# Kernel tuning notes

Measured on AMD Instinct MI355X. Metric: run time of the kernel, lower is better.

The kernel has to match this reference:

```python
import jax, jax.numpy as jnp
import numpy as np

N_OUT, N_CONS, N_AGE = 7, 20, 15
H = 256
B, T = 64, 365
D_ECO = N_CONS + N_AGE          # 35: eco+age feed the shared eco LSTM
D_BR = 1 + 3 + H                # 260: init + 3 age cols + eco LSTM output


def setup_inputs() -> dict:
    key = jax.random.key(0)
    ks = jax.random.split(key, 24)
    s = 0.05
    w = lambda k, shape: (jax.random.normal(k, shape, jnp.float32) * s)
    z = lambda shape: jnp.zeros(shape, jnp.float32)
    return {
        "inputs": jax.random.normal(ks[0], (B, T, N_CONS + N_OUT + N_AGE), jnp.float32),
        # shared eco LSTM (n_lstm_eco = 1)
        "eco_Wk": w(ks[1], (D_ECO, 4 * H)), "eco_Wr": w(ks[2], (H, 4 * H)), "eco_b": z((4 * H,)),
        # per-output data LSTMs (tanh)
        "data_Wk": w(ks[3], (N_OUT, D_BR, 4 * H)), "data_Wr": w(ks[4], (N_OUT, H, 4 * H)), "data_b": z((N_OUT, 4 * H)),
        # per-output attention LSTMs (activation='sigmoid')
        "att_Wk": w(ks[5], (N_OUT, D_BR, 4 * H)), "att_Wr": w(ks[6], (N_OUT, H, 4 * H)), "att_b": z((N_OUT, 4 * H)),
        # per-output tsOut LSTMs (return last state)
        "ts_Wk": w(ks[7], (N_OUT, H, 4 * H)), "ts_Wr": w(ks[8], (N_OUT, H, 4 * H)), "ts_b": z((N_OUT, 4 * H)),
        # per-output dense heads
        "d1_W": w(ks[9], (N_OUT, H, 256)), "d1_b": z((N_OUT, 256)),
        "d2_W": w(ks[10], (N_OUT, 256, 64)), "d2_b": z((N_OUT, 64)),
        "df_W": w(ks[11], (N_OUT, 64 + 3, 1)), "df_b": z((N_OUT, 1)),
    }


def _lstm(x, Wk, Wr, b, act):
    """Keras-style LSTM. x: [B,T,D]. Returns (all hidden [B,T,H], last hidden [B,H])."""
    Bc = x.shape[0]
    Hc = Wr.shape[0]
    xW = jnp.einsum('btd,dg->btg', x, Wk) + b      # precompute input projections

    def step(carry, xt):
        h, c = carry
        zi, zf, zg, zo = jnp.split(xt + h @ Wr, 4, axis=-1)  # Keras gate order i,f,c,o
        c = jax.nn.sigmoid(zf) * c + jax.nn.sigmoid(zi) * act(zg)
        h = jax.nn.sigmoid(zo) * act(c)
        return (h, c), h

    init = (jnp.zeros((Bc, Hc), x.dtype), jnp.zeros((Bc, Hc), x.dtype))
    (hT, _), hs = jax.lax.scan(step, init, jnp.swapaxes(xW, 0, 1))
    return jnp.swapaxes(hs, 0, 1), hT


def _branch(init_i, age_i, dWk, dWr, db, aWk, aWr, ab, tWk, tWr, tb, w1, b1, w2, b2, wf, bf, x_ecos):
    # init_i: [B,T,1], age_i: [B,T,3], x_ecos: [B,T,H] (shared)
    cur_input = jnp.concatenate([init_i, age_i, x_ecos], axis=-1)  # [B,T,260]
    data_hs, _ = _lstm(cur_input, dWk, dWr, db, jnp.tanh)
    att_hs, _ = _lstm(cur_input, aWk, aWr, ab, jax.nn.sigmoid)     # activation='sigmoid'
    _, h_last = _lstm(data_hs * att_hs, tWk, tWr, tb, jnp.tanh)    # return_sequences=False
    h = jax.nn.relu(h_last @ w1 + b1)
    h = jax.nn.relu(h @ w2 + b2)
    h = jnp.concatenate([h, cur_input[:, -1, 1:4]], axis=-1)       # append last-step age cols
    out = h @ wf + bf + cur_input[:, -1, :1]                       # residual add of last init
    return out  # [B,1]


def reference(inputs, eco_Wk, eco_Wr, eco_b, data_Wk, data_Wr, data_b,
              att_Wk, att_Wr, att_b, ts_Wk, ts_Wr, ts_b,
              d1_W, d1_b, d2_W, d2_b, df_W, df_b):
    x_init = inputs[:, :, N_CONS:N_CONS + N_OUT]                       # [B,T,7]
    x_age = inputs[:, :, N_CONS + N_OUT:N_CONS + N_OUT + N_AGE]        # [B,T,15]
    x_eco = inputs[:, :, :N_CONS]                                      # [B,T,20]

    x_ecos, _ = _lstm(jnp.concatenate([x_eco, x_age], axis=-1), eco_Wk, eco_Wr, eco_b, jnp.tanh)  # [B,T,256]

    init_i = jnp.moveaxis(x_init, 2, 0)[..., None]                     # [7,B,T,1]
    i_idx = jnp.arange(N_OUT)
    age_cols = jnp.stack([jnp.zeros_like(i_idx), i_idx + 1, i_idx + 8], axis=1)  # [7,3]
    age_i = jnp.moveaxis(x_age[:, :, age_cols], 2, 0)                  # [7,B,T,3]

    outs = jax.vmap(_branch, in_axes=(0,) * 17 + (None,))(
        init_i, age_i, data_Wk, data_Wr, data_b, att_Wk, att_Wr, att_b,
        ts_Wk, ts_Wr, ts_b, d1_W, d1_b, d2_W, d2_b, df_W, df_b, x_ecos)  # [7,B,1]
    return jnp.transpose(outs[:, :, 0])  # [B,7]
```

## Files before the change

### kernel.cpp

```cpp
#include <hip/hip_runtime.h>


#define TT 365
#define RE 4
#define RS 4

typedef short bf16x8 __attribute__((ext_vector_type(8)));
typedef float f32x4 __attribute__((ext_vector_type(4)));

__device__ __forceinline__ float b2f(unsigned short u) {
  union { unsigned u32; float f; } v; v.u32 = ((unsigned)u) << 16; return v.f;
}
__device__ __forceinline__ unsigned short f2b(float f) {
  union { float f; unsigned u32; } v; v.f = f;
  unsigned u = v.u32;
  u = u + 0x7FFFu + ((u >> 16) & 1u);
  return (unsigned short)(u >> 16);
}
__device__ __forceinline__ float sigf(float x) { return 1.0f / (1.0f + __expf(-x)); }
__device__ __forceinline__ float tanh_(float x) { return 2.0f / (1.0f + __expf(-2.0f * x)) - 1.0f; }

__device__ __forceinline__ unsigned long long ld64(const unsigned long long* p) {
  return __hip_atomic_load(p, __ATOMIC_RELAXED, __HIP_MEMORY_SCOPE_AGENT);
}
// ... 51 lines not shown
  __syncthreads();
  for (int e = tid; e < 8192; e += 256) {
    int col2 = e >> 5, ks = e & 31;
    dst[(size_t)kb * 32768 + (cc * 256 + col2) * 32 + ks] = f2b(ls[ks * 261 + col2]);
  }
}

__global__ __launch_bounds__(256) void k1_ecoxw(const float* __restrict__ inputs,
    const float* __restrict__ eco_Wk, const float* __restrict__ eco_b,
    unsigned short* __restrict__ xw_eco)
{
  __shared__ float Asl[64 * 35];
  __shared__ float Bsl[35 * 256];
  const int tg = blockIdx.x, ct = blockIdx.y, tid = threadIdx.x;
  for (int i = tid; i < 64 * 35; i += 256) {
    int b = i / 35, k = i - b * 35;
    int col = (k < 20) ? k : (k + 7);
    Asl[i] = inputs[((size_t)b * TT + tg) * 42 + col];
  }
  for (int i = tid; i < 35 * 256; i += 256) {
    int k = i >> 8, c = i & 255;
    Bsl[i] = eco_Wk[(size_t)k * 1024 + ct * 256 + c];
  }
  __syncthreads();
  const float bias = eco_b[ct * 256 + tid];
  for (int r = 0; r < 64; ++r) {
    float s = bias;
    #pragma unroll
    for (int k = 0; k < 35; ++k) s += Asl[r * 35 + k] * Bsl[k * 256 + tid];
    xw_eco[((size_t)tg * 64 + r) * 1024 + ct * 256 + tid] = f2b(s);
  }
}

__global__ __launch_bounds__(256, 1) void kP(
    const unsigned short* __restrict__ wr_swz,
    const unsigned short* __restrict__ wk_da,
    const unsigned short* __restrict__ wk_ts,
    const unsigned short* __restrict__ xw_eco,
    const float* __restrict__ inputs,
    const float* __restrict__ data_Wk, const float* __restrict__ att_Wk,
    const float* __restrict__ data_b, const float* __restrict__ att_b,
    const float* __restrict__ ts_b,
    unsigned long long* __restrict__ hE,
    unsigned long long* __restrict__ hD,
    unsigned long long* __restrict__ hsD,
    unsigned long long* __restrict__ hsA,
    unsigned long long* __restrict__ h2,
    unsigned* __restrict__ hDf, unsigned* __restrict__ h2f,
    float* __restrict__ h_last)
{
  __shared__ __align__(16) unsigned char smem[160256];
  const int tid = threadIdx.x;
  const int widx = blockIdx.x;
  const int lane = tid & 63, w = tid >> 6, c = lane & 15, grp = lane >> 4;

  if (widx < 16) {
    unsigned short* WR = (unsigned short*)smem;
    unsigned short* Hs = (unsigned short*)(smem + 81920);
    float* zsh = (float*)(smem + 102400);
    float* cst = (float*)(smem + 119296);
    const int wg = widx >> 1, bg = widx & 1;
    const unsigned short* wr_g = wr_swz + (size_t)wg * 32768;
    for (int i = tid * 8; i < 32768; i += 2048) {
      int kb = i >> 12; int rr = i & 4095; int col = rr >> 5; int ks = rr & 31;
      *(uint4*)&WR[(kb * 128 + col) * 40 + ks] = *(const uint4*)&wr_g[i];
    }
    for (int i = tid; i < 1024; i += 256) cst[i] = 0.0f;

    int xoff[16];
    #pragma unroll
    for (int rt = 0; rt < 2; ++rt)
      #pragma unroll
      for (int ct = 0; ct < 2; ++ct)
        #pragma unroll
        for (int rg = 0; rg < 4; ++rg)
          xoff[(rt * 2 + ct) * 4 + rg] =
              (bg * 32 + rt * 16 + grp * 4 + rg) * 1024 + w * 256 + wg * 32 + ct * 16 + c;
    unsigned short xv[16], xn[16];
    #pragma unroll
    for (int i = 0; i < 16; ++i) xv[i] = xw_eco[xoff[i]];
    __syncthreads();

    for (int t = 0; t < TT; ++t) {
      if (t + 1 > RE && tid < 112) {
        while ((int)ld32(&hDf[tid]) < t + 1 - RE) __builtin_amdgcn_s_sleep(2);
      }
      {
        const unsigned long long* hb = hE + (size_t)(t % RE) * 8192;
        unsigned long long v[16];
        #pragma unroll
        for (int i = 0; i < 16; ++i) {
          int m = tid + i * 256;
          v[i] = ld64(&hb[(bg * 32 + (m >> 7)) * 128 + (m & 127)]);
        }
        const unsigned tagv = (unsigned)t;
        int tries = 0;
        while (true) {
          unsigned pend = 0u;
          #pragma unroll
          for (int i = 0; i < 16; ++i)
            pend |= ((unsigned)(v[i] >> 32) != tagv) ? (1u << i) : 0u;
          if (!pend) break;
          if (++tries > 8) __builtin_amdgcn_s_sleep(1);
          #pragma unroll
          for (int i = 0; i < 16; ++i)
            if (pend & (1u << i)) {
              int m = tid + i * 256;
              v[i] = ld64(&hb[(bg * 32 + (m >> 7)) * 128 + (m & 127)]);
            }
        }
        #pragma unroll
        for (int i = 0; i < 16; ++i) {
          int m = tid + i * 256, row = m >> 7, kp = m & 127;
          *(unsigned int*)&Hs[((kp >> 4) * 32 + row) * 40 + 2 * (kp & 15)] = (unsigned int)v[i];
        }
      }
      __syncthreads();
      f32x4 acc[4];
      #pragma unroll
      for (int i = 0; i < 4; ++i)
        #pragma unroll
        for (int rg = 0; rg < 4; ++rg) acc[i][rg] = b2f(xv[i * 4 + rg]);
      if (t + 1 < TT) {
        const unsigned short* xw1 = xw_eco + (size_t)(t + 1) * 65536;
        #pragma unroll
        for (int i = 0; i < 16; ++i) xn[i] = xw1[xoff[i]];
      }
      #pragma unroll
      for (int kb = 0; kb < 8; ++kb) {
        bf16x8 a0 = *(const bf16x8*)&Hs[(kb * 32 + c) * 40 + grp * 8];
        bf16x8 a1 = *(const bf16x8*)&Hs[(kb * 32 + 16 + c) * 40 + grp * 8];
        bf16x8 b0 = *(const bf16x8*)&WR[(kb * 128 + w * 32 + c) * 40 + grp * 8];
        bf16x8 b1 = *(const bf16x8*)&WR[(kb * 128 + w * 32 + 16 + c) * 40 + grp * 8];
        acc[0] = __builtin_amdgcn_mfma_f32_16x16x32_bf16(a0, b0, acc[0], 0, 0, 0);
        acc[1] = __builtin_amdgcn_mfma_f32_16x16x32_bf16(a0, b1, acc[1], 0, 0, 0);
        acc[2] = __builtin_amdgcn_mfma_f32_16x16x32_bf16(a1, b0, acc[2], 0, 0, 0);
        acc[3] = __builtin_amdgcn_mfma_f32_16x16x32_bf16(a1, b1, acc[3], 0, 0, 0);
      }
      #pragma unroll
      for (int i = 0; i < 4; ++i) {
        int rt = i >> 1, ct = i & 1;
        #pragma unroll
        for (int rg = 0; rg < 4; ++rg)
          zsh[(rt * 16 + grp * 4 + rg) * 132 + w * 32 + ct * 16 + c] = acc[i][rg];
      }
      __syncthreads();
      {
        int row = tid >> 3, hq8 = tid & 7;
        float4 zi = *(const float4*)&zsh[row * 132 +      hq8 * 4];
        float4 zf = *(const float4*)&zsh[row * 132 + 32 + hq8 * 4];
        float4 zg = *(const float4*)&zsh[row * 132 + 64 + hq8 * 4];
        float4 zo = *(const float4*)&zsh[row * 132 + 96 + hq8 * 4];
        float4 c0 = *(const float4*)&cst[row * 32 + hq8 * 4];
        float cn0 = sigf(zf.x) * c0.x + sigf(zi.x) * tanh_(zg.x);
        float cn1 = sigf(zf.y) * c0.y + sigf(zi.y) * tanh_(zg.y);
        float cn2 = sigf(zf.z) * c0.z + sigf(zi.z) * tanh_(zg.z);
        float cn3 = sigf(zf.w) * c0.w + sigf(zi.w) * tanh_(zg.w);
        float hv0 = sigf(zo.x) * tanh_(cn0);
        float hv1 = sigf(zo.y) * tanh_(cn1);
        float hv2 = sigf(zo.z) * tanh_(cn2);
        float hv3 = sigf(zo.w) * tanh_(cn3);
        *(float4*)&cst[row * 32 + hq8 * 4] = make_float4(cn0, cn1, cn2, cn3);
        unsigned long long* ho = hE + (size_t)((t + 1) % RE) * 8192
                               + (bg * 32 + row) * 128 + wg * 16 + hq8 * 2;
        st64(&ho[0], tag2(t + 1, hv0, hv1));
        st64(&ho[1], tag2(t + 1, hv2, hv3));
      }
      __syncthreads();
      #pragma unroll
      for (int i = 0; i < 16; ++i) xv[i] = xn[i];
    }
  } else if (widx < 128) {
    unsigned short* WR = (unsigned short*)smem;
    unsigned short* Hs = (unsigned short*)(smem + 81920);
    float* zsh = (float*)(smem + 122880);
    float* a_sp = (float*)(smem + 156672);
    float* b_sp = (float*)(smem + 157696);
    float* bias_s = (float*)(smem + 159744);
    const int q = widx - 16, l1 = q >> 3, colwg = q & 7, br = l1 >> 1;
    const bool act_sig = (l1 & 1);
    const unsigned short* wr_g = wr_swz + ((size_t)(1 + l1) * 8 + colwg) * 32768;
    for (int i = tid * 8; i < 32768; i += 2048) {
      int kb = i >> 12; int rr = i & 4095; int col = rr >> 5; int ks = rr & 31;
      *(uint4*)&WR[(kb * 128 + col) * 40 + ks] = *(const uint4*)&wr_g[i];
    }
    bf16x8 wkf[16];
    const unsigned short* wk = wk_da + (size_t)l1 * 262144;
    #pragma unroll
    for (int kb = 0; kb < 8; ++kb)
      #pragma unroll
      for (int ct = 0; ct < 2; ++ct) {
        int col = w * 256 + colwg * 32 + ct * 16 + c;
        wkf[kb * 2 + ct] = *(const bf16x8*)&wk[kb * 32768 + col * 32 + grp * 8];
      }
    const float* spWk = (act_sig ? att_Wk : data_Wk) + (size_t)br * 266240;
    for (int i = tid; i < 512; i += 256) {
      int j = i >> 7, colL = i & 127;
      int gcol = (colL >> 5) * 256 + colwg * 32 + (colL & 31);
      b_sp[i] = spWk[(size_t)j * 1024 + gcol];
    }
    if (tid < 128) {
      int gcol = (tid >> 5) * 256 + colwg * 32 + (tid & 31);
      bias_s[tid] = (act_sig ? att_b : data_b)[br * 1024 + gcol];
    }
    float creg[8];
    #pragma unroll
    for (int j = 0; j < 8; ++j) creg[j] = 0.0f;
    unsigned long long* hDl = hD + (size_t)l1 * 2 * 8192;
    unsigned long long* ring = (act_sig ? hsA : hsD) + (size_t)br * RS * 8192;
    __syncthreads();

    for (int t = 0; t < TT; ++t) {
      if (t + 1 > RS && tid < 16) {
        while ((int)ld32(&h2f[br * 16 + tid]) < t + 1 - RS) __builtin_amdgcn_s_sleep(2);
      }
      if (tid < 64) {
        const float* ip = inputs + ((size_t)tid * TT + t) * 42;
        a_sp[tid * 4 + 0] = ip[20 + br];
        a_sp[tid * 4 + 1] = ip[27];
        a_sp[tid * 4 + 2] = ip[27 + br + 1];
        a_sp[tid * 4 + 3] = ip[27 + br + 8];
      }
      const unsigned long long* he = hE + (size_t)((t + 1) % RE) * 8192;
      const unsigned long long* ho = hDl + (size_t)(t & 1) * 8192;
      unsigned long long ve[32], vh[32];
      #pragma unroll
      for (int i = 0; i < 32; ++i) ve[i] = ld64(&he[tid + i * 256]);
      #pragma unroll
      for (int i = 0; i < 32; ++i) vh[i] = ld64(&ho[tid + i * 256]);
      {
        const unsigned tagv = (unsigned)(t + 1);
        int tries = 0;
        while (true) {
          unsigned long long pend = 0ull;
          #pragma unroll
          for (int i = 0; i < 32; ++i)
            pend |= ((unsigned)(ve[i] >> 32) != tagv) ? (1ull << i) : 0ull;
          if (!pend) break;
          if (++tries > 8) __builtin_amdgcn_s_sleep(1);
          #pragma unroll
          for (int i = 0; i < 32; ++i)
            if (pend & (1ull << i)) ve[i] = ld64(&he[tid + i * 256]);
        }
      }
      #pragma unroll
      for (int i = 0; i < 32; ++i) {
        int m = tid + i * 256, row = m >> 7, kp = m & 127;
        *(unsigned int*)&Hs[((kp >> 4) * 64 + row) * 40 + 2 * (kp & 15)] = (unsigned int)ve[i];
      }
      __syncthreads();
      f32x4 acc[8] = {};
      #pragma unroll
      for (int kb = 0; kb < 8; ++kb) {
        bf16x8 a[4];
        #pragma unroll
        for (int rt = 0; rt < 4; ++rt)
          a[rt] = *(const bf16x8*)&Hs[(kb * 64 + rt * 16 + c) * 40 + grp * 8];
        #pragma unroll
        for (int rt = 0; rt < 4; ++rt)
          #pragma unroll
          for (int ct = 0; ct < 2; ++ct)
            acc[rt * 2 + ct] = __builtin_amdgcn_mfma_f32_16x16x32_bf16(a[rt], wkf[kb * 2 + ct], acc[rt * 2 + ct], 0, 0, 0);
      }
      #pragma unroll
      for (int i = 0; i < 8; ++i) {
        int rt = i >> 1, ct2 = i & 1;
        #pragma unroll
        for (int rg = 0; rg < 4; ++rg) {
          int row = rt * 16 + grp * 4 + rg;
          int colL = w * 32 + ct2 * 16 + c;
          acc[i][rg] += bias_s[colL]
                      + a_sp[row * 4 + 0] * b_sp[colL]       + a_sp[row * 4 + 1] * b_sp[128 + colL]
                      + a_sp[row * 4 + 2] * b_sp[256 + colL] + a_sp[row * 4 + 3] * b_sp[384 + colL];
        }
      }
      {
        const unsigned tagv = (unsigned)t;
        int tries = 0;
        while (true) {
          unsigned long long pend = 0ull;
          #pragma unroll
          for (int i = 0; i < 32; ++i)
            pend |= ((unsigned)(vh[i] >> 32) != tagv) ? (1ull << i) : 0ull;
          if (!pend) break;
          if (++tries > 8) __builtin_amdgcn_s_sleep(1);
          #pragma unroll
          for (int i = 0; i < 32; ++i)
            if (pend & (1ull << i)) vh[i] = ld64(&ho[tid + i * 256]);
        }
      }
      __syncthreads();
      #pragma unroll
      for (int i = 0; i < 32; ++i) {
        int m = tid + i * 256, row = m >> 7, kp = m & 127;
        *(unsigned int*)&Hs[((kp >> 4) * 64 + row) * 40 + 2 * (kp & 15)] = (unsigned int)vh[i];
      }
      __syncthreads();
      #pragma unroll
      for (int kb = 0; kb < 8; ++kb) {
        bf16x8 a[4]; bf16x8 b[2];
        #pragma unroll
        for (int rt = 0; rt < 4; ++rt)
          a[rt] = *(const bf16x8*)&Hs[(kb * 64 + rt * 16 + c) * 40 + grp * 8];
        #pragma unroll
        for (int ct = 0; ct < 2; ++ct)
          b[ct] = *(const bf16x8*)&WR[(kb * 128 + w * 32 + ct * 16 + c) * 40 + grp * 8];
        #pragma unroll
        for (int rt = 0; rt < 4; ++rt)
          #pragma unroll
          for (int ct = 0; ct < 2; ++ct)
            acc[rt * 2 + ct] = __builtin_amdgcn_mfma_f32_16x16x32_bf16(a[rt], b[ct], acc[rt * 2 + ct], 0, 0, 0);
      }
      #pragma unroll
      for (int i = 0; i < 8; ++i) {
        int rt = i >> 1, ct2 = i & 1;
        #pragma unroll
        for (int rg = 0; rg < 4; ++rg)
          zsh[(rt * 16 + grp * 4 + rg) * 132 + w * 32 + ct2 * 16 + c] = acc[i][rg];
      }
      __syncthreads();
      {
        unsigned long long* hon = hDl + (size_t)((t + 1) & 1) * 8192;
        unsigned long long* rs = ring + (size_t)(t % RS) * 8192;
        #pragma unroll
        for (int it = 0; it < 2; ++it) {
          int m = tid + it * 256, row = m >> 3, hq8 = m & 7;
          float4 zi = *(const float4*)&zsh[row * 132 +      hq8 * 4];
          float4 zf = *(const float4*)&zsh[row * 132 + 32 + hq8 * 4];
          float4 zg = *(const float4*)&zsh[row * 132 + 64 + hq8 * 4];
          float4 zo = *(const float4*)&zsh[row * 132 + 96 + hq8 * 4];
          float g0 = act_sig ? sigf(zg.x) : tanh_(zg.x);
          float g1 = act_sig ? sigf(zg.y) : tanh_(zg.y);
          float g2 = act_sig ? sigf(zg.z) : tanh_(zg.z);
          float g3 = act_sig ? sigf(zg.w) : tanh_(zg.w);
          float cn0 = sigf(zf.x) * creg[it * 4 + 0] + sigf(zi.x) * g0;
          float cn1 = sigf(zf.y) * creg[it * 4 + 1] + sigf(zi.y) * g1;
          float cn2 = sigf(zf.z) * creg[it * 4 + 2] + sigf(zi.z) * g2;
          float cn3 = sigf(zf.w) * creg[it * 4 + 3] + sigf(zi.w) * g3;
          float hv0 = sigf(zo.x) * (act_sig ? sigf(cn0) : tanh_(cn0));
          float hv1 = sigf(zo.y) * (act_sig ? sigf(cn1) : tanh_(cn1));
          float hv2 = sigf(zo.z) * (act_sig ? sigf(cn2) : tanh_(cn2));
          float hv3 = sigf(zo.w) * (act_sig ? sigf(cn3) : tanh_(cn3));
          creg[it * 4 + 0] = cn0; creg[it * 4 + 1] = cn1;
          creg[it * 4 + 2] = cn2; creg[it * 4 + 3] = cn3;
          int kp = colwg * 16 + hq8 * 2;
          unsigned long long w0 = tag2(t + 1, hv0, hv1);
          unsigned long long w1 = tag2(t + 1, hv2, hv3);
          st64(&hon[row * 128 + kp], w0);
          st64(&hon[row * 128 + kp + 1], w1);
          st64(&rs[row * 128 + kp], w0);
          st64(&rs[row * 128 + kp + 1], w1);
        }
      }
      __builtin_amdgcn_s_waitcnt(0);
      __syncthreads();
      if (tid == 0) st32(&hDf[q], (unsigned)(t + 1));
    }
  } else {
    unsigned short* WR = (unsigned short*)smem;
    unsigned short* Hs = (unsigned short*)(smem + 81920);
    float* zsh = (float*)(smem + 102400);
    float* bias_s = (float*)(smem + 119296);
    const int r = widx - 128, d = r >> 4, sub = r & 15, colwg = sub >> 1, bg = sub & 1;
    const unsigned short* wr_g = wr_swz + ((size_t)(15 + d) * 8 + colwg) * 32768;
    for (int i = tid * 8; i < 32768; i += 2048) {
      int kb = i >> 12; int rr = i & 4095; int col = rr >> 5; int ks = rr & 31;
      *(uint4*)&WR[(kb * 128 + col) * 40 + ks] = *(const uint4*)&wr_g[i];
    }
    bf16x8 wkf[16];
    const unsigned short* wk = wk_ts + (size_t)d * 262144;
    #pragma unroll
    for (int kb = 0; kb < 8; ++kb)
      #pragma unroll
      for (int ct = 0; ct < 2; ++ct) {
        int col = w * 256 + colwg * 32 + ct * 16 + c;
        wkf[kb * 2 + ct] = *(const bf16x8*)&wk[kb * 32768 + col * 32 + grp * 8];
      }
    if (tid < 128) {
      int gcol = (tid >> 5) * 256 + colwg * 32 + (tid & 31);
      bias_s[tid] = ts_b[d * 1024 + gcol];
    }
    float creg[4] = {0.0f, 0.0f, 0.0f, 0.0f};
    const unsigned long long* rD = hsD + (size_t)d * RS * 8192;
    const unsigned long long* rA = hsA + (size_t)d * RS * 8192;
    unsigned long long* h2d = h2 + (size_t)d * 2 * 8192;
    __syncthreads();

    for (int t = 0; t < TT; ++t) {
      const unsigned long long* sd = rD + (size_t)(t % RS) * 8192;
      const unsigned long long* sa = rA + (size_t)(t % RS) * 8192;
      const unsigned long long* ho = h2d + (size_t)(t & 1) * 8192;
      unsigned long long vd[16], va[16], vh[16];
      int idx16[16];
      #pragma unroll
      for (int i = 0; i < 16; ++i) {
        int m = tid + i * 256;
        idx16[i] = (bg * 32 + (m >> 7)) * 128 + (m & 127);
      }
      #pragma unroll
      for (int i = 0; i < 16; ++i) vd[i] = ld64(&sd[idx16[i]]);
      #pragma unroll
      for (int i = 0; i < 16; ++i) va[i] = ld64(&sa[idx16[i]]);
      #pragma unroll
      for (int i = 0; i < 16; ++i) vh[i] = ld64(&ho[idx16[i]]);
      {
        const unsigned tagv = (unsigned)(t + 1);
        int tries = 0;
        while (true) {
          unsigned pend = 0u;
          #pragma unroll
          for (int i = 0; i < 16; ++i) {
            pend |= ((unsigned)(vd[i] >> 32) != tagv) ? (1u << i) : 0u;
            pend |= ((unsigned)(va[i] >> 32) != tagv) ? (0x10000u << i) : 0u;
          }
          if (!pend) break;
          if (++tries > 8) __builtin_amdgcn_s_sleep(1);
          #pragma unroll
          for (int i = 0; i < 16; ++i) {
            if (pend & (1u << i)) vd[i] = ld64(&sd[idx16[i]]);
            if (pend & (0x10000u << i)) va[i] = ld64(&sa[idx16[i]]);
          }
        }
      }
      #pragma unroll
      for (int i = 0; i < 16; ++i) {
        int m = tid + i * 256, row = m >> 7, kp = m & 127;
        unsigned dl = (unsigned)vd[i], al = (unsigned)va[i];
        float p0 = b2f((unsigned short)dl) * b2f((unsigned short)al);
        float p1 = b2f((unsigned short)(dl >> 16)) * b2f((unsigned short)(al >> 16));
        unsigned pv = (unsigned)f2b(p0) | ((unsigned)f2b(p1) << 16);
        *(unsigned int*)&Hs[((kp >> 4) * 32 + row) * 40 + 2 * (kp & 15)] = pv;
      }
      __syncthreads();
      f32x4 acc[4] = {};
      #pragma unroll
      for (int kb = 0; kb < 8; ++kb) {
        bf16x8 a0 = *(const bf16x8*)&Hs[(kb * 32 + c) * 40 + grp * 8];
        bf16x8 a1 = *(const bf16x8*)&Hs[(kb * 32 + 16 + c) * 40 + grp * 8];
        acc[0] = __builtin_amdgcn_mfma_f32_16x16x32_bf16(a0, wkf[kb * 2 + 0], acc[0], 0, 0, 0);
        acc[1] = __builtin_amdgcn_mfma_f32_16x16x32_bf16(a0, wkf[kb * 2 + 1], acc[1], 0, 0, 0);
        acc[2] = __builtin_amdgcn_mfma_f32_16x16x32_bf16(a1, wkf[kb * 2 + 0], acc[2], 0, 0, 0);
        acc[3] = __builtin_amdgcn_mfma_f32_16x16x32_bf16(a1, wkf[kb * 2 + 1], acc[3], 0, 0, 0);
      }
      #pragma unroll
      for (int i = 0; i < 4; ++i) {
        int ct2 = i & 1;
        #pragma unroll
        for (int rg = 0; rg < 4; ++rg)
          acc[i][rg] += bias_s[w * 32 + ct2 * 16 + c];
      }
      {
        const unsigned tagv = (unsigned)t;
        int tries = 0;
        while (true) {
          unsigned pend = 0u;
          #pragma unroll
          for (int i = 0; i < 16; ++i)
            pend |= ((unsigned)(vh[i] >> 32) != tagv) ? (1u << i) : 0u;
          if (!pend) break;
          if (++tries > 8) __builtin_amdgcn_s_sleep(1);
          #pragma unroll
          for (int i = 0; i < 16; ++i)
            if (pend & (1u << i)) vh[i] = ld64(&ho[idx16[i]]);
        }
      }
      __syncthreads();
      #pragma unroll
      for (int i = 0; i < 16; ++i) {
        int m = tid + i * 256, row = m >> 7, kp = m & 127;
        *(unsigned int*)&Hs[((kp >> 4) * 32 + row) * 40 + 2 * (kp & 15)] = (unsigned int)vh[i];
      }
      __syncthreads();
      #pragma unroll
      for (int kb = 0; kb < 8; ++kb) {
        bf16x8 a0 = *(const bf16x8*)&Hs[(kb * 32 + c) * 40 + grp * 8];
        bf16x8 a1 = *(const bf16x8*)&Hs[(kb * 32 + 16 + c) * 40 + grp * 8];
        bf16x8 b0 = *(const bf16x8*)&WR[(kb * 128 + w * 32 + c) * 40 + grp * 8];
        bf16x8 b1 = *(const bf16x8*)&WR[(kb * 128 + w * 32 + 16 + c) * 40 + grp * 8];
        acc[0] = __builtin_amdgcn_mfma_f32_16x16x32_bf16(a0, b0, acc[0], 0, 0, 0);
        acc[1] = __builtin_amdgcn_mfma_f32_16x16x32_bf16(a0, b1, acc[1], 0, 0, 0);
        acc[2] = __builtin_amdgcn_mfma_f32_16x16x32_bf16(a1, b0, acc[2], 0, 0, 0);
        acc[3] = __builtin_amdgcn_mfma_f32_16x16x32_bf16(a1, b1, acc[3], 0, 0, 0);
      }
      #pragma unroll
      for (int i = 0; i < 4; ++i) {
        int rt = i >> 1, ct2 = i & 1;
        #pragma unroll
        for (int rg = 0; rg < 4; ++rg)
          zsh[(rt * 16 + grp * 4 + rg) * 132 + w * 32 + ct2 * 16 + c] = acc[i][rg];
      }
      __syncthreads();
      {
        int row = tid >> 3, hq8 = tid & 7;
        float4 zi = *(const float4*)&zsh[row * 132 +      hq8 * 4];
        float4 zf = *(const float4*)&zsh[row * 132 + 32 + hq8 * 4];
        float4 zg = *(const float4*)&zsh[row * 132 + 64 + hq8 * 4];
        float4 zo = *(const float4*)&zsh[row * 132 + 96 + hq8 * 4];
        float cn0 = sigf(zf.x) * creg[0] + sigf(zi.x) * tanh_(zg.x);
        float cn1 = sigf(zf.y) * creg[1] + sigf(zi.y) * tanh_(zg.y);
        float cn2 = sigf(zf.z) * creg[2] + sigf(zi.z) * tanh_(zg.z);
        float cn3 = sigf(zf.w) * creg[3] + sigf(zi.w) * tanh_(zg.w);
        float hv0 = sigf(zo.x) * tanh_(cn0);
        float hv1 = sigf(zo.y) * tanh_(cn1);
        float hv2 = sigf(zo.z) * tanh_(cn2);
        float hv3 = sigf(zo.w) * tanh_(cn3);
        creg[0] = cn0; creg[1] = cn1; creg[2] = cn2; creg[3] = cn3;
        unsigned long long* hn = h2d + (size_t)((t + 1) & 1) * 8192
                               + (bg * 32 + row) * 128 + colwg * 16 + hq8 * 2;
        st64(&hn[0], tag2(t + 1, hv0, hv1));
        st64(&hn[1], tag2(t + 1, hv2, hv3));
        if (t == TT - 1) {
          *(float4*)&h_last[(size_t)d * 16384 + (bg * 32 + row) * 256 + colwg * 32 + hq8 * 4]
              = make_float4(hv0, hv1, hv2, hv3);
        }
      }
      __builtin_amdgcn_s_waitcnt(0);
      __syncthreads();
      if (tid == 0) st32(&h2f[d * 16 + sub], (unsigned)(t + 1));
    }
  }
}

__global__ __launch_bounds__(256) void k7_d1(const float* __restrict__ h_last,
    const float* __restrict__ d1_W, const float* __restrict__ d1_b, float* __restrict__ d1o)
{
  __shared__ float Asl[64 * 256];
  __shared__ float Bsl[256 * 64];
  const int nt = blockIdx.x, br = blockIdx.y, tid = threadIdx.x;
  const float* hl = h_last + (size_t)br * 16384;
  for (int i = tid; i < 16384; i += 256) Asl[i] = hl[i];
  const float* wp = d1_W + (size_t)br * 65536 + nt * 64;
  for (int i = tid; i < 16384; i += 256) {
    int k = i >> 6, cl = i & 63;
    Bsl[i] = wp[(size_t)k * 256 + cl];
  }
  __syncthreads();
  const int cl = tid & 63, rq = tid >> 6;
  float s[16];
  const float bias = d1_b[br * 256 + nt * 64 + cl];
  #pragma unroll
  for (int i = 0; i < 16; ++i) s[i] = bias;
  for (int k = 0; k < 256; ++k) {
    float bv = Bsl[k * 64 + cl];
    #pragma unroll
    for (int i = 0; i < 16; ++i) s[i] += Asl[(rq * 16 + i) * 256 + k] * bv;
  }
  #pragma unroll
  for (int i = 0; i < 16; ++i)
    d1o[(size_t)br * 16384 + (rq * 16 + i) * 256 + nt * 64 + cl] = fmaxf(s[i], 0.0f);
}

// ... 49 lines not shown
  const float* att_Wk  = (const float*)d_in[7];
  const float* att_Wr  = (const float*)d_in[8];
  const float* att_b   = (const float*)d_in[9];
  const float* ts_Wk   = (const float*)d_in[10];
  const float* ts_Wr   = (const float*)d_in[11];
  const float* ts_b    = (const float*)d_in[12];
  const float* d1_W    = (const float*)d_in[13];
  const float* d1_b    = (const float*)d_in[14];
  const float* d2_W    = (const float*)d_in[15];
  const float* d2_b    = (const float*)d_in[16];
  const float* df_W    = (const float*)d_in[17];
  const float* df_b    = (const float*)d_in[18];

  char* ws = (char*)d_ws;
  size_t off = 0;
  auto take = [&](size_t bytes) -> void* {
    void* p = ws + off;
    off += (bytes + 255) & ~(size_t)255;
    return p;
  };
  unsigned short* wr_swz = (unsigned short*)take((size_t)22 * 262144 * 2);
  unsigned short* wk_da  = (unsigned short*)take((size_t)14 * 262144 * 2);
  unsigned short* wk_ts  = (unsigned short*)take((size_t)7  * 262144 * 2);
  unsigned short* xw_eco = (unsigned short*)take((size_t)TT * 65536 * 2);
  float*          h_last = (float*)take((size_t)7 * 16384 * 4);
  float*          d1o    = (float*)take((size_t)7 * 16384 * 4);
  size_t sync_begin = off;
  unsigned long long* hE  = (unsigned long long*)take((size_t)RE * 8192 * 8);
  unsigned long long* hD  = (unsigned long long*)take((size_t)14 * 2 * 8192 * 8);
  unsigned long long* hsD = (unsigned long long*)take((size_t)7 * RS * 8192 * 8);
  unsigned long long* hsA = (unsigned long long*)take((size_t)7 * RS * 8192 * 8);
  unsigned long long* h2  = (unsigned long long*)take((size_t)7 * 2 * 8192 * 8);
  unsigned* hDf = (unsigned*)take(112 * 4);
  unsigned* h2f = (unsigned*)take(112 * 4);
  size_t sync_bytes = off - sync_begin;
  if (off > ws_size) return;

  hipMemsetAsync(ws + sync_begin, 0, sync_bytes, stream);
  k0a_wr<<<dim3(8, 8, 22), 256, 0, stream>>>(eco_Wr, data_Wr, att_Wr, ts_Wr, wr_swz);
  k0b_wk<<<dim3(4, 8, 21), 256, 0, stream>>>(data_Wk, att_Wk, ts_Wk, wk_da, wk_ts);
  k1_ecoxw<<<dim3(TT, 4), 256, 0, stream>>>(inputs, eco_Wk, eco_b, xw_eco);
  kP<<<240, 256, 0, stream>>>(wr_swz, wk_da, wk_ts, xw_eco, inputs,
                              data_Wk, att_Wk, data_b, att_b, ts_b,
                              hE, hD, hsD, hsA, h2, hDf, h2f, h_last);
  k7_d1<<<dim3(4, 7), 256, 0, stream>>>(h_last, d1_W, d1_b, d1o);
  k8_head<<<7, 256, 0, stream>>>(d1o, d2_W, d2_b, df_W, df_b, inputs, (float*)d_out);
}
```

Before: 3.904 ms.

## Merge batch-half workgroups into 512-thread blocks in persistent LSTM kernel

The persistent recurrence kernel now runs 512-thread workgroups. Each block covers both 32-row batch halves that were previously handled by separate blocks, so each recurrent weight slice is loaded into shared memory once instead of twice. The grid shrinks from 240 to 176 blocks, and the per-step readiness flags for the ts LSTM drop from 16 to 8 per branch. The eco cell state moves into registers and one block barrier per eco step is dropped. In exchange, each block carries more waves and larger barrier groups, which may lengthen per-step barrier latency on the serial critical path.

```diff
diff --git a/kernel.cpp b/kernel.cpp
--- a/kernel.cpp
+++ b/kernel.cpp
@@ -107,7 +107,7 @@
   }
 }
 
-__global__ __launch_bounds__(256, 1) void kP(
+__global__ __launch_bounds__(512, 2) void kP(
     const unsigned short* __restrict__ wr_swz,
     const unsigned short* __restrict__ wk_da,
     const unsigned short* __restrict__ wk_ts,
@@ -127,21 +127,20 @@
   __shared__ __align__(16) unsigned char smem[160256];
   const int tid = threadIdx.x;
   const int widx = blockIdx.x;
-  const int lane = tid & 63, w = tid >> 6, c = lane & 15, grp = lane >> 4;
-
-  if (widx < 16) {
+  const int lane = tid & 63, w = (tid >> 6) & 3, c = lane & 15, grp = lane >> 4;
+  const int half = tid >> 8, tid256 = tid & 255;
+  const int crow = tid >> 3, chq = tid & 7;
+
+  if (widx < 8) {
     unsigned short* WR = (unsigned short*)smem;
     unsigned short* Hs = (unsigned short*)(smem + 81920);
-    float* zsh = (float*)(smem + 102400);
-    float* cst = (float*)(smem + 119296);
-    const int wg = widx >> 1, bg = widx & 1;
+    float* zsh = (float*)(smem + 122880);
+    const int wg = widx;
     const unsigned short* wr_g = wr_swz + (size_t)wg * 32768;
-    for (int i = tid * 8; i < 32768; i += 2048) {
+    for (int i = tid * 8; i < 32768; i += 4096) {
       int kb = i >> 12; int rr = i & 4095; int col = rr >> 5; int ks = rr & 31;
       *(uint4*)&WR[(kb * 128 + col) * 40 + ks] = *(const uint4*)&wr_g[i];
     }
-    for (int i = tid; i < 1024; i += 256) cst[i] = 0.0f;
-
     int xoff[16];
     #pragma unroll
     for (int rt = 0; rt < 2; ++rt)
@@ -150,10 +149,11 @@
         #pragma unroll
         for (int rg = 0; rg < 4; ++rg)
           xoff[(rt * 2 + ct) * 4 + rg] =
-              (bg * 32 + rt * 16 + grp * 4 + rg) * 1024 + w * 256 + wg * 32 + ct * 16 + c;
+              (half * 32 + rt * 16 + grp * 4 + rg) * 1024 + w * 256 + wg * 32 + ct * 16 + c;
     unsigned short xv[16], xn[16];
     #pragma unroll
     for (int i = 0; i < 16; ++i) xv[i] = xw_eco[xoff[i]];
+    float cs0 = 0.0f, cs1 = 0.0f, cs2 = 0.0f, cs3 = 0.0f;
     __syncthreads();
 
     for (int t = 0; t < TT; ++t) {
@@ -165,8 +165,8 @@
         unsigned long long v[16];
         #pragma unroll
         for (int i = 0; i < 16; ++i) {
-          int m = tid + i * 256;
-          v[i] = ld64(&hb[(bg * 32 + (m >> 7)) * 128 + (m & 127)]);
+          int m = tid256 + i * 256;
+          v[i] = ld64(&hb[(half * 32 + (m >> 7)) * 128 + (m & 127)]);
         }
         const unsigned tagv = (unsigned)t;
         int tries = 0;
@@ -180,14 +180,15 @@
           #pragma unroll
           for (int i = 0; i < 16; ++i)
             if (pend & (1u << i)) {
-              int m = tid + i * 256;
-              v[i] = ld64(&hb[(bg * 32 + (m >> 7)) * 128 + (m & 127)]);
+              int m = tid256 + i * 256;
+              v[i] = ld64(&hb[(half * 32 + (m >> 7)) * 128 + (m & 127)]);
             }
         }
         #pragma unroll
         for (int i = 0; i < 16; ++i) {
-          int m = tid + i * 256, row = m >> 7, kp = m & 127;
-          *(unsigned int*)&Hs[((kp >> 4) * 32 + row) * 40 + 2 * (kp & 15)] = (unsigned int)v[i];
+          int m = tid256 + i * 256, rl = m >> 7, kp = m & 127;
+          *(unsigned int*)&Hs[half * 10240 + ((kp >> 4) * 32 + rl) * 40 + 2 * (kp & 15)]
+              = (unsigned int)v[i];
         }
       }
       __syncthreads();
@@ -203,8 +204,8 @@
       }
       #pragma unroll
       for (int kb = 0; kb < 8; ++kb) {
-        bf16x8 a0 = *(const bf16x8*)&Hs[(kb * 32 + c) * 40 + grp * 8];
-        bf16x8 a1 = *(const bf16x8*)&Hs[(kb * 32 + 16 + c) * 40 + grp * 8];
+        bf16x8 a0 = *(const bf16x8*)&Hs[half * 10240 + (kb * 32 + c) * 40 + grp * 8];
+        bf16x8 a1 = *(const bf16x8*)&Hs[half * 10240 + (kb * 32 + 16 + c) * 40 + grp * 8];
         bf16x8 b0 = *(const bf16x8*)&WR[(kb * 128 + w * 32 + c) * 40 + grp * 8];
         bf16x8 b1 = *(const bf16x8*)&WR[(kb * 128 + w * 32 + 16 + c) * 40 + grp * 8];
         acc[0] = __builtin_amdgcn_mfma_f32_16x16x32_bf16(a0, b0, acc[0], 0, 0, 0);
@@ -217,45 +218,42 @@
         int rt = i >> 1, ct = i & 1;
         #pragma unroll
         for (int rg = 0; rg < 4; ++rg)
-          zsh[(rt * 16 + grp * 4 + rg) * 132 + w * 32 + ct * 16 + c] = acc[i][rg];
+          zsh[(half * 32 + rt * 16 + grp * 4 + rg) * 132 + w * 32 + ct * 16 + c] = acc[i][rg];
       }
       __syncthreads();
       {
-        int row = tid >> 3, hq8 = tid & 7;
-        float4 zi = *(const float4*)&zsh[row * 132 +      hq8 * 4];
-        float4 zf = *(const float4*)&zsh[row * 132 + 32 + hq8 * 4];
-        float4 zg = *(const float4*)&zsh[row * 132 + 64 + hq8 * 4];
-        float4 zo = *(const float4*)&zsh[row * 132 + 96 + hq8 * 4];
-        float4 c0 = *(const float4*)&cst[row * 32 + hq8 * 4];
-        float cn0 = sigf(zf.x) * c0.x + sigf(zi.x) * tanh_(zg.x);
-        float cn1 = sigf(zf.y) * c0.y + sigf(zi.y) * tanh_(zg.y);
-        float cn2 = sigf(zf.z) * c0.z + sigf(zi.z) * tanh_(zg.z);
-        float cn3 = sigf(zf.w) * c0.w + sigf(zi.w) * tanh_(zg.w);
+        float4 zi = *(const float4*)&zsh[crow * 132 +      chq * 4];
+        float4 zf = *(const float4*)&zsh[crow * 132 + 32 + chq * 4];
+        float4 zg = *(const float4*)&zsh[crow * 132 + 64 + chq * 4];
+        float4 zo = *(const float4*)&zsh[crow * 132 + 96 + chq * 4];
+        float cn0 = sigf(zf.x) * cs0 + sigf(zi.x) * tanh_(zg.x);
+        float cn1 = sigf(zf.y) * cs1 + sigf(zi.y) * tanh_(zg.y);
+        float cn2 = sigf(zf.z) * cs2 + sigf(zi.z) * tanh_(zg.z);
+        float cn3 = sigf(zf.w) * cs3 + sigf(zi.w) * tanh_(zg.w);
         float hv0 = sigf(zo.x) * tanh_(cn0);
         float hv1 = sigf(zo.y) * tanh_(cn1);
         float hv2 = sigf(zo.z) * tanh_(cn2);
         float hv3 = sigf(zo.w) * tanh_(cn3);
-        *(float4*)&cst[row * 32 + hq8 * 4] = make_float4(cn0, cn1, cn2, cn3);
+        cs0 = cn0; cs1 = cn1; cs2 = cn2; cs3 = cn3;
         unsigned long long* ho = hE + (size_t)((t + 1) % RE) * 8192
-                               + (bg * 32 + row) * 128 + wg * 16 + hq8 * 2;
+                               + crow * 128 + wg * 16 + chq * 2;
         st64(&ho[0], tag2(t + 1, hv0, hv1));
         st64(&ho[1], tag2(t + 1, hv2, hv3));
       }
-      __syncthreads();
       #pragma unroll
       for (int i = 0; i < 16; ++i) xv[i] = xn[i];
     }
-  } else if (widx < 128) {
+  } else if (widx < 120) {
     unsigned short* WR = (unsigned short*)smem;
     unsigned short* Hs = (unsigned short*)(smem + 81920);
     float* zsh = (float*)(smem + 122880);
     float* a_sp = (float*)(smem + 156672);
     float* b_sp = (float*)(smem + 157696);
     float* bias_s = (float*)(smem + 159744);
-    const int q = widx - 16, l1 = q >> 3, colwg = q & 7, br = l1 >> 1;
+    const int q = widx - 8, l1 = q >> 3, colwg = q & 7, br = l1 >> 1;
     const bool act_sig = (l1 & 1);
     const unsigned short* wr_g = wr_swz + ((size_t)(1 + l1) * 8 + colwg) * 32768;
-    for (int i = tid * 8; i < 32768; i += 2048) {
+    for (int i = tid * 8; i < 32768; i += 4096) {
       int kb = i >> 12; int rr = i & 4095; int col = rr >> 5; int ks = rr & 31;
       *(uint4*)&WR[(kb * 128 + col) * 40 + ks] = *(const uint4*)&wr_g[i];
     }
@@ -269,25 +267,23 @@
         wkf[kb * 2 + ct] = *(const bf16x8*)&wk[kb * 32768 + col * 32 + grp * 8];
       }
     const float* spWk = (act_sig ? att_Wk : data_Wk) + (size_t)br * 266240;
-    for (int i = tid; i < 512; i += 256) {
-      int j = i >> 7, colL = i & 127;
+    {
+      int j = tid >> 7, colL = tid & 127;
       int gcol = (colL >> 5) * 256 + colwg * 32 + (colL & 31);
-      b_sp[i] = spWk[(size_t)j * 1024 + gcol];
+      b_sp[tid] = spWk[(size_t)j * 1024 + gcol];
     }
     if (tid < 128) {
       int gcol = (tid >> 5) * 256 + colwg * 32 + (tid & 31);
       bias_s[tid] = (act_sig ? att_b : data_b)[br * 1024 + gcol];
     }
-    float creg[8];
-    #pragma unroll
-    for (int j = 0; j < 8; ++j) creg[j] = 0.0f;
+    float creg[4] = {0.0f, 0.0f, 0.0f, 0.0f};
     unsigned long long* hDl = hD + (size_t)l1 * 2 * 8192;
     unsigned long long* ring = (act_sig ? hsA : hsD) + (size_t)br * RS * 8192;
     __syncthreads();
 
     for (int t = 0; t < TT; ++t) {
-      if (t + 1 > RS && tid < 16) {
-        while ((int)ld32(&h2f[br * 16 + tid]) < t + 1 - RS) __builtin_amdgcn_s_sleep(2);
+      if (t + 1 > RS && tid < 8) {
+        while ((int)ld32(&h2f[br * 8 + tid]) < t + 1 - RS) __builtin_amdgcn_s_sleep(2);
       }
       if (tid < 64) {
         const float* ip = inputs + ((size_t)tid * TT + t) * 42;
@@ -298,51 +294,58 @@
       }
       const unsigned long long* he = hE + (size_t)((t + 1) % RE) * 8192;
       const unsigned long long* ho = hDl + (size_t)(t & 1) * 8192;
-      unsigned long long ve[32], vh[32];
-      #pragma unroll
-      for (int i = 0; i < 32; ++i) ve[i] = ld64(&he[tid + i * 256]);
-      #pragma unroll
-      for (int i = 0; i < 32; ++i) vh[i] = ld64(&ho[tid + i * 256]);
+      unsigned long long ve[16], vh[16];
+      #pragma unroll
+      for (int i = 0; i < 16; ++i) {
+        int m = tid256 + i * 256;
+        int idx = (half * 32 + (m >> 7)) * 128 + (m & 127);
+        ve[i] = ld64(&he[idx]);
+        vh[i] = ld64(&ho[idx]);
+      }
       {
         const unsigned tagv = (unsigned)(t + 1);
         int tries = 0;
         while (true) {
-          unsigned long long pend = 0ull;
-          #pragma unroll
-          for (int i = 0; i < 32; ++i)
-            pend |= ((unsigned)(ve[i] >> 32) != tagv) ? (1ull << i) : 0ull;
+          unsigned pend = 0u;
+          #pragma unroll
+          for (int i = 0; i < 16; ++i)
+            pend |= ((unsigned)(ve[i] >> 32) != tagv) ? (1u << i) : 0u;
           if (!pend) break;
           if (++tries > 8) __builtin_amdgcn_s_sleep(1);
           #pragma unroll
-          for (int i = 0; i < 32; ++i)
-            if (pend & (1ull << i)) ve[i] = ld64(&he[tid + i * 256]);
-        }
-      }
-      #pragma unroll
-      for (int i = 0; i < 32; ++i) {
-        int m = tid + i * 256, row = m >> 7, kp = m & 127;
-        *(unsigned int*)&Hs[((kp >> 4) * 64 + row) * 40 + 2 * (kp & 15)] = (unsigned int)ve[i];
-      }
-      __syncthreads();
-      f32x4 acc[8] = {};
+          for (int i = 0; i < 16; ++i)
+            if (pend & (1u << i)) {
+              int m = tid256 + i * 256;
+              ve[i] = ld64(&he[(half * 32 + (m >> 7)) * 128 + (m & 127)]);
+            }
+        }
+      }
+      #pragma unroll
+      for (int i = 0; i < 16; ++i) {
+        int m = tid256 + i * 256, rl = m >> 7, kp = m & 127;
+        *(unsigned int*)&Hs[((kp >> 4) * 64 + half * 32 + rl) * 40 + 2 * (kp & 15)]
+            = (unsigned int)ve[i];
+      }
+      __syncthreads();
+      f32x4 acc[4] = {};
       #pragma unroll
       for (int kb = 0; kb < 8; ++kb) {
-        bf16x8 a[4];
-        #pragma unroll
-        for (int rt = 0; rt < 4; ++rt)
-          a[rt] = *(const bf16x8*)&Hs[(kb * 64 + rt * 16 + c) * 40 + grp * 8];
-        #pragma unroll
-        for (int rt = 0; rt < 4; ++rt)
+        bf16x8 a[2];
+        #pragma unroll
+        for (int rt = 0; rt < 2; ++rt)
+          a[rt] = *(const bf16x8*)&Hs[(kb * 64 + half * 32 + rt * 16 + c) * 40 + grp * 8];
+        #pragma unroll
+        for (int rt = 0; rt < 2; ++rt)
           #pragma unroll
           for (int ct = 0; ct < 2; ++ct)
             acc[rt * 2 + ct] = __builtin_amdgcn_mfma_f32_16x16x32_bf16(a[rt], wkf[kb * 2 + ct], acc[rt * 2 + ct], 0, 0, 0);
       }
       #pragma unroll
-      for (int i = 0; i < 8; ++i) {
+      for (int i = 0; i < 4; ++i) {
         int rt = i >> 1, ct2 = i & 1;
         #pragma unroll
         for (int rg = 0; rg < 4; ++rg) {
-          int row = rt * 16 + grp * 4 + rg;
+          int row = half * 32 + rt * 16 + grp * 4 + rg;
           int colL = w * 32 + ct2 * 16 + c;
           acc[i][rg] += bias_s[colL]
                       + a_sp[row * 4 + 0] * b_sp[colL]       + a_sp[row * 4 + 1] * b_sp[128 + colL]
@@ -353,79 +356,78 @@
         const unsigned tagv = (unsigned)t;
         int tries = 0;
         while (true) {
-          unsigned long long pend = 0ull;
-          #pragma unroll
-          for (int i = 0; i < 32; ++i)
-            pend |= ((unsigned)(vh[i] >> 32) != tagv) ? (1ull << i) : 0ull;
+          unsigned pend = 0u;
+          #pragma unroll
+          for (int i = 0; i < 16; ++i)
+            pend |= ((unsigned)(vh[i] >> 32) != tagv) ? (1u << i) : 0u;
           if (!pend) break;
           if (++tries > 8) __builtin_amdgcn_s_sleep(1);
           #pragma unroll
-          for (int i = 0; i < 32; ++i)
-            if (pend & (1ull << i)) vh[i] = ld64(&ho[tid + i * 256]);
-        }
-      }
-      __syncthreads();
-      #pragma unroll
-      for (int i = 0; i < 32; ++i) {
-        int m = tid + i * 256, row = m >> 7, kp = m & 127;
-        *(unsigned int*)&Hs[((kp >> 4) * 64 + row) * 40 + 2 * (kp & 15)] = (unsigned int)vh[i];
+          for (int i = 0; i < 16; ++i)
+            if (pend & (1u << i)) {
+              int m = tid256 + i * 256;
+              vh[i] = ld64(&ho[(half * 32 + (m >> 7)) * 128 + (m & 127)]);
+            }
+        }
+      }
+      __syncthreads();
+      #pragma unroll
+      for (int i = 0; i < 16; ++i) {
+        int m = tid256 + i * 256, rl = m >> 7, kp = m & 127;
+        *(unsigned int*)&Hs[((kp >> 4) * 64 + half * 32 + rl) * 40 + 2 * (kp & 15)]
+            = (unsigned int)vh[i];
       }
       __syncthreads();
       #pragma unroll
       for (int kb = 0; kb < 8; ++kb) {
-        bf16x8 a[4]; bf16x8 b[2];
-        #pragma unroll
-        for (int rt = 0; rt < 4; ++rt)
-          a[rt] = *(const bf16x8*)&Hs[(kb * 64 + rt * 16 + c) * 40 + grp * 8];
+        bf16x8 a[2]; bf16x8 b[2];
+        #pragma unroll
+        for (int rt = 0; rt < 2; ++rt)
+          a[rt] = *(const bf16x8*)&Hs[(kb * 64 + half * 32 + rt * 16 + c) * 40 + grp * 8];
         #pragma unroll
         for (int ct = 0; ct < 2; ++ct)
           b[ct] = *(const bf16x8*)&WR[(kb * 128 + w * 32 + ct * 16 + c) * 40 + grp * 8];
         #pragma unroll
-        for (int rt = 0; rt < 4; ++rt)
+        for (int rt = 0; rt < 2; ++rt)
           #pragma unroll
           for (int ct = 0; ct < 2; ++ct)
             acc[rt * 2 + ct] = __builtin_amdgcn_mfma_f32_16x16x32_bf16(a[rt], b[ct], acc[rt * 2 + ct], 0, 0, 0);
       }
       #pragma unroll
-      for (int i = 0; i < 8; ++i) {
+      for (int i = 0; i < 4; ++i) {
         int rt = i >> 1, ct2 = i & 1;
         #pragma unroll
         for (int rg = 0; rg < 4; ++rg)
-          zsh[(rt * 16 + grp * 4 + rg) * 132 + w * 32 + ct2 * 16 + c] = acc[i][rg];
+          zsh[(half * 32 + rt * 16 + grp * 4 + rg) * 132 + w * 32 + ct2 * 16 + c] = acc[i][rg];
       }
       __syncthreads();
       {
         unsigned long long* hon = hDl + (size_t)((t + 1) & 1) * 8192;
         unsigned long long* rs = ring + (size_t)(t % RS) * 8192;
-        #pragma unroll
-        for (int it = 0; it < 2; ++it) {
-          int m = tid + it * 256, row = m >> 3, hq8 = m & 7;
-          float4 zi = *(const float4*)&zsh[row * 132 +      hq8 * 4];
-          float4 zf = *(const float4*)&zsh[row * 132 + 32 + hq8 * 4];
-          float4 zg = *(const float4*)&zsh[row * 132 + 64 + hq8 * 4];
-          float4 zo = *(const float4*)&zsh[row * 132 + 96 + hq8 * 4];
-          float g0 = act_sig ? sigf(zg.x) : tanh_(zg.x);
-          float g1 = act_sig ? sigf(zg.y) : tanh_(zg.y);
-          float g2 = act_sig ? sigf(zg.z) : tanh_(zg.z);
-          float g3 = act_sig ? sigf(zg.w) : tanh_(zg.w);
-          float cn0 = sigf(zf.x) * creg[it * 4 + 0] + sigf(zi.x) * g0;
-          float cn1 = sigf(zf.y) * creg[it * 4 + 1] + sigf(zi.y) * g1;
-          float cn2 = sigf(zf.z) * creg[it * 4 + 2] + sigf(zi.z) * g2;
-          float cn3 = sigf(zf.w) * creg[it * 4 + 3] + sigf(zi.w) * g3;
-          float hv0 = sigf(zo.x) * (act_sig ? sigf(cn0) : tanh_(cn0));
-          float hv1 = sigf(zo.y) * (act_sig ? sigf(cn1) : tanh_(cn1));
-          float hv2 = sigf(zo.z) * (act_sig ? sigf(cn2) : tanh_(cn2));
-          float hv3 = sigf(zo.w) * (act_sig ? sigf(cn3) : tanh_(cn3));
-          creg[it * 4 + 0] = cn0; creg[it * 4 + 1] = cn1;
-          creg[it * 4 + 2] = cn2; creg[it * 4 + 3] = cn3;
-          int kp = colwg * 16 + hq8 * 2;
-          unsigned long long w0 = tag2(t + 1, hv0, hv1);
-          unsigned long long w1 = tag2(t + 1, hv2, hv3);
-          st64(&hon[row * 128 + kp], w0);
-          st64(&hon[row * 128 + kp + 1], w1);
-          st64(&rs[row * 128 + kp], w0);
-          st64(&rs[row * 128 + kp + 1], w1);
-        }
+        float4 zi = *(const float4*)&zsh[crow * 132 +      chq * 4];
+        float4 zf = *(const float4*)&zsh[crow * 132 + 32 + chq * 4];
+        float4 zg = *(const float4*)&zsh[crow * 132 + 64 + chq * 4];
+        float4 zo = *(const float4*)&zsh[crow * 132 + 96 + chq * 4];
+        float g0 = act_sig ? sigf(zg.x) : tanh_(zg.x);
+        float g1 = act_sig ? sigf(zg.y) : tanh_(zg.y);
+        float g2 = act_sig ? sigf(zg.z) : tanh_(zg.z);
+        float g3 = act_sig ? sigf(zg.w) : tanh_(zg.w);
+        float cn0 = sigf(zf.x) * creg[0] + sigf(zi.x) * g0;
+        float cn1 = sigf(zf.y) * creg[1] + sigf(zi.y) * g1;
+        float cn2 = sigf(zf.z) * creg[2] + sigf(zi.z) * g2;
+        float cn3 = sigf(zf.w) * creg[3] + sigf(zi.w) * g3;
+        float hv0 = sigf(zo.x) * (act_sig ? sigf(cn0) : tanh_(cn0));
+        float hv1 = sigf(zo.y) * (act_sig ? sigf(cn1) : tanh_(cn1));
+        float hv2 = sigf(zo.z) * (act_sig ? sigf(cn2) : tanh_(cn2));
+        float hv3 = sigf(zo.w) * (act_sig ? sigf(cn3) : tanh_(cn3));
+        creg[0] = cn0; creg[1] = cn1; creg[2] = cn2; creg[3] = cn3;
+        int kp = colwg * 16 + chq * 2;
+        unsigned long long w0 = tag2(t + 1, hv0, hv1);
+        unsigned long long w1 = tag2(t + 1, hv2, hv3);
+        st64(&hon[crow * 128 + kp], w0);
+        st64(&hon[crow * 128 + kp + 1], w1);
+        st64(&rs[crow * 128 + kp], w0);
+        st64(&rs[crow * 128 + kp + 1], w1);
       }
       __builtin_amdgcn_s_waitcnt(0);
       __syncthreads();
@@ -434,11 +436,11 @@
   } else {
     unsigned short* WR = (unsigned short*)smem;
     unsigned short* Hs = (unsigned short*)(smem + 81920);
-    float* zsh = (float*)(smem + 102400);
-    float* bias_s = (float*)(smem + 119296);
-    const int r = widx - 128, d = r >> 4, sub = r & 15, colwg = sub >> 1, bg = sub & 1;
+    float* zsh = (float*)(smem + 122880);
+    float* bias_s = (float*)(smem + 156672);
+    const int r = widx - 120, d = r >> 3, colwg = r & 7;
     const unsigned short* wr_g = wr_swz + ((size_t)(15 + d) * 8 + colwg) * 32768;
-    for (int i = tid * 8; i < 32768; i += 2048) {
+    for (int i = tid * 8; i < 32768; i += 4096) {
       int kb = i >> 12; int rr = i & 4095; int col = rr >> 5; int ks = rr & 31;
       *(uint4*)&WR[(kb * 128 + col) * 40 + ks] = *(const uint4*)&wr_g[i];
     }
@@ -469,8 +471,8 @@
       int idx16[16];
       #pragma unroll
       for (int i = 0; i < 16; ++i) {
-        int m = tid + i * 256;
-        idx16[i] = (bg * 32 + (m >> 7)) * 128 + (m & 127);
+        int m = tid256 + i * 256;
+        idx16[i] = (half * 32 + (m >> 7)) * 128 + (m & 127);
       }
       #pragma unroll
       for (int i = 0; i < 16; ++i) vd[i] = ld64(&sd[idx16[i]]);
@@ -499,19 +501,19 @@
       }
       #pragma unroll
       for (int i = 0; i < 16; ++i) {
-        int m = tid + i * 256, row = m >> 7, kp = m & 127;
+        int m = tid256 + i * 256, rl = m >> 7, kp = m & 127;
         unsigned dl = (unsigned)vd[i], al = (unsigned)va[i];
         float p0 = b2f((unsigned short)dl) * b2f((unsigned short)al);
         float p1 = b2f((unsigned short)(dl >> 16)) * b2f((unsigned short)(al >> 16));
         unsigned pv = (unsigned)f2b(p0) | ((unsigned)f2b(p1) << 16);
-        *(unsigned int*)&Hs[((kp >> 4) * 32 + row) * 40 + 2 * (kp & 15)] = pv;
+        *(unsigned int*)&Hs[((kp >> 4) * 64 + half * 32 + rl) * 40 + 2 * (kp & 15)] = pv;
       }
       __syncthreads();
       f32x4 acc[4] = {};
       #pragma unroll
       for (int kb = 0; kb < 8; ++kb) {
-        bf16x8 a0 = *(const bf16x8*)&Hs[(kb * 32 + c) * 40 + grp * 8];
-        bf16x8 a1 = *(const bf16x8*)&Hs[(kb * 32 + 16 + c) * 40 + grp * 8];
+        bf16x8 a0 = *(const bf16x8*)&Hs[(kb * 64 + half * 32 + c) * 40 + grp * 8];
+        bf16x8 a1 = *(const bf16x8*)&Hs[(kb * 64 + half * 32 + 16 + c) * 40 + grp * 8];
         acc[0] = __builtin_amdgcn_mfma_f32_16x16x32_bf16(a0, wkf[kb * 2 + 0], acc[0], 0, 0, 0);
         acc[1] = __builtin_amdgcn_mfma_f32_16x16x32_bf16(a0, wkf[kb * 2 + 1], acc[1], 0, 0, 0);
         acc[2] = __builtin_amdgcn_mfma_f32_16x16x32_bf16(a1, wkf[kb * 2 + 0], acc[2], 0, 0, 0);
@@ -542,14 +544,15 @@
       __syncthreads();
       #pragma unroll
       for (int i = 0; i < 16; ++i) {
-        int m = tid + i * 256, row = m >> 7, kp = m & 127;
-        *(unsigned int*)&Hs[((kp >> 4) * 32 + row) * 40 + 2 * (kp & 15)] = (unsigned int)vh[i];
+        int m = tid256 + i * 256, rl = m >> 7, kp = m & 127;
+        *(unsigned int*)&Hs[((kp >> 4) * 64 + half * 32 + rl) * 40 + 2 * (kp & 15)]
+            = (unsigned int)vh[i];
       }
       __syncthreads();
       #pragma unroll
       for (int kb = 0; kb < 8; ++kb) {
-        bf16x8 a0 = *(const bf16x8*)&Hs[(kb * 32 + c) * 40 + grp * 8];
-        bf16x8 a1 = *(const bf16x8*)&Hs[(kb * 32 + 16 + c) * 40 + grp * 8];
+        bf16x8 a0 = *(const bf16x8*)&Hs[(kb * 64 + half * 32 + c) * 40 + grp * 8];
+        bf16x8 a1 = *(const bf16x8*)&Hs[(kb * 64 + half * 32 + 16 + c) * 40 + grp * 8];
         bf16x8 b0 = *(const bf16x8*)&WR[(kb * 128 + w * 32 + c) * 40 + grp * 8];
         bf16x8 b1 = *(const bf16x8*)&WR[(kb * 128 + w * 32 + 16 + c) * 40 + grp * 8];
         acc[0] = __builtin_amdgcn_mfma_f32_16x16x32_bf16(a0, b0, acc[0], 0, 0, 0);
@@ -562,15 +565,14 @@
         int rt = i >> 1, ct2 = i & 1;
         #pragma unroll
         for (int rg = 0; rg < 4; ++rg)
-          zsh[(rt * 16 + grp * 4 + rg) * 132 + w * 32 + ct2 * 16 + c] = acc[i][rg];
+          zsh[(half * 32 + rt * 16 + grp * 4 + rg) * 132 + w * 32 + ct2 * 16 + c] = acc[i][rg];
       }
       __syncthreads();
       {
-        int row = tid >> 3, hq8 = tid & 7;
-        float4 zi = *(const float4*)&zsh[row * 132 +      hq8 * 4];
-        float4 zf = *(const float4*)&zsh[row * 132 + 32 + hq8 * 4];
-        float4 zg = *(const float4*)&zsh[row * 132 + 64 + hq8 * 4];
-        float4 zo = *(const float4*)&zsh[row * 132 + 96 + hq8 * 4];
+        float4 zi = *(const float4*)&zsh[crow * 132 +      chq * 4];
+        float4 zf = *(const float4*)&zsh[crow * 132 + 32 + chq * 4];
+        float4 zg = *(const float4*)&zsh[crow * 132 + 64 + chq * 4];
+        float4 zo = *(const float4*)&zsh[crow * 132 + 96 + chq * 4];
         float cn0 = sigf(zf.x) * creg[0] + sigf(zi.x) * tanh_(zg.x);
         float cn1 = sigf(zf.y) * creg[1] + sigf(zi.y) * tanh_(zg.y);
         float cn2 = sigf(zf.z) * creg[2] + sigf(zi.z) * tanh_(zg.z);
@@ -581,17 +583,17 @@
         float hv3 = sigf(zo.w) * tanh_(cn3);
         creg[0] = cn0; creg[1] = cn1; creg[2] = cn2; creg[3] = cn3;
         unsigned long long* hn = h2d + (size_t)((t + 1) & 1) * 8192
-                               + (bg * 32 + row) * 128 + colwg * 16 + hq8 * 2;
+                               + crow * 128 + colwg * 16 + chq * 2;
         st64(&hn[0], tag2(t + 1, hv0, hv1));
         st64(&hn[1], tag2(t + 1, hv2, hv3));
         if (t == TT - 1) {
-          *(float4*)&h_last[(size_t)d * 16384 + (bg * 32 + row) * 256 + colwg * 32 + hq8 * 4]
+          *(float4*)&h_last[(size_t)d * 16384 + crow * 256 + colwg * 32 + chq * 4]
               = make_float4(hv0, hv1, hv2, hv3);
         }
       }
       __builtin_amdgcn_s_waitcnt(0);
       __syncthreads();
-      if (tid == 0) st32(&h2f[d * 16 + sub], (unsigned)(t + 1));
+      if (tid == 0) st32(&h2f[d * 8 + colwg], (unsigned)(t + 1));
     }
   }
 }
@@ -707,7 +709,7 @@
   unsigned long long* hsA = (unsigned long long*)take((size_t)7 * RS * 8192 * 8);
   unsigned long long* h2  = (unsigned long long*)take((size_t)7 * 2 * 8192 * 8);
   unsigned* hDf = (unsigned*)take(112 * 4);
-  unsigned* h2f = (unsigned*)take(112 * 4);
+  unsigned* h2f = (unsigned*)take(56 * 4);
   size_t sync_bytes = off - sync_begin;
   if (off > ws_size) return;
 
@@ -715,7 +717,7 @@
   k0a_wr<<<dim3(8, 8, 22), 256, 0, stream>>>(eco_Wr, data_Wr, att_Wr, ts_Wr, wr_swz);
   k0b_wk<<<dim3(4, 8, 21), 256, 0, stream>>>(data_Wk, att_Wk, ts_Wk, wk_da, wk_ts);
   k1_ecoxw<<<dim3(TT, 4), 256, 0, stream>>>(inputs, eco_Wk, eco_b, xw_eco);
-  kP<<<240, 256, 0, stream>>>(wr_swz, wk_da, wk_ts, xw_eco, inputs,
+  kP<<<176, 512, 0, stream>>>(wr_swz, wk_da, wk_ts, xw_eco, inputs,
                               data_Wk, att_Wk, data_b, att_b, ts_b,
                               hE, hD, hsD, hsA, h2, hDf, h2f, h_last);
   k7_d1<<<dim3(4, 7), 256, 0, stream>>>(h_last, d1_W, d1_b, d1o);
```

Measured after the change: 4.906 ms. 25.7% more time.
